# Kernel tuning notes

Hardware: AMD Instinct MI355X
Metric: run time of the kernel (lower is better)

Reference implementation:

```python
import jax, jax.numpy as jnp
import numpy as np

B, N, H, D, L = 4, 1024, 8, 256, 4
SVD, NSP = 16, 512
DK = D // H
EPS = 1e-6


def setup_inputs() -> dict:
    key = jax.random.key(0)
    ks = jax.random.split(key, 40)
    p = {}
    p["x"] = jax.random.normal(ks[0], (B, N, D), jnp.float32)
    p["in_degrees"] = jax.random.randint(ks[1], (N,), 0, N)
    p["out_degrees"] = jax.random.randint(ks[2], (N,), 0, N)
    p["spatial_pos"] = jax.random.randint(ks[3], (N, N), 0, NSP)
    p["svd_emb"] = jax.random.normal(ks[4], (N, 2 * SVD), jnp.float32)
    # embedding tables (padding_idx=0 -> zero row)
    p["in_deg_emb"] = (0.02 * jax.random.normal(ks[5], (N, D), jnp.float32)).at[0].set(0.0)
    p["out_deg_emb"] = (0.02 * jax.random.normal(ks[6], (N, D), jnp.float32)).at[0].set(0.0)
    p["spatial_emb"] = (0.02 * jax.random.normal(ks[7], (NSP, H), jnp.float32)).at[0].set(0.0)
    # SVD linear (stored [in, out]; y = x @ W + b)
    p["W_svd"] = 0.02 * jax.random.normal(ks[8], (2 * SVD, D), jnp.float32)
    p["b_svd"] = jnp.zeros((D,), jnp.float32)
    # per-layer stacked transformer params
    names = ["Wq", "Wk", "Wv", "Wa", "W1", "W2"]
    for i, nm in enumerate(names):
        p[nm] = 0.05 * jax.random.normal(ks[9 + i], (L, D, D), jnp.float32)
    for nm in ["bq", "bk", "bv", "ba", "b1", "b2", "ln1_b", "ln2_b"]:
        p[nm] = jnp.zeros((L, D), jnp.float32)
    p["ln1_g"] = jnp.ones((L, D), jnp.float32)
    p["ln2_g"] = jnp.ones((L, D), jnp.float32)
    return p


def _ln(x, g, b):
    mu = jnp.mean(x, axis=-1, keepdims=True)
    var = jnp.mean(jnp.square(x - mu), axis=-1, keepdims=True)
    return (x - mu) * jax.lax.rsqrt(var + EPS) * g + b


def _forward(x, svd_emb, W_svd, b_svd, in_deg_emb, out_deg_emb, spatial_emb,
             Wq, bq, Wk, bk, Wv, bv, Wa, ba, ln1_g, ln1_b,
             W1, b1, W2, b2, ln2_g, ln2_b,
             in_degrees, out_degrees, spatial_pos):
    # node-level: degree embeddings ([N,D] broadcasts over batch)
    x = x + in_deg_emb[in_degrees] + out_deg_emb[out_degrees]
    # node-level: SVD embedding (deterministic sign = +1 -> concat(u, -v))
    pos = jnp.concatenate([svd_emb[:, :SVD], -svd_emb[:, SVD:]], axis=-1)
    x = x + pos @ W_svd + b_svd
    # attention-level spatial bias: [N,N,H] -> [H,N,N], broadcast over batch
    attn_bias = jnp.transpose(spatial_emb[spatial_pos], (2, 0, 1))
    scale = 1.0 / jnp.sqrt(jnp.asarray(DK, x.dtype))

    def body(h, params):
        wq, bq_, wk, bk_, wv, bv_, wa, ba_, g1, b1_, w1, bb1, w2, bb2, g2, b2_ = params
        q = (h @ wq + bq_).reshape(B, N, H, DK)
        k = (h @ wk + bk_).reshape(B, N, H, DK)
        v = (h @ wv + bv_).reshape(B, N, H, DK)
        # scores [B,H,N,N] + spatial bias [H,N,N]
        scores = jnp.einsum('bqhd,bkhd->bhqk', q, k) * scale + attn_bias
        attn = jax.nn.softmax(scores, axis=-1)
        o = jnp.einsum('bhqk,bkhd->bqhd', attn, v).reshape(B, N, D)
        h = _ln(h + o @ wa + ba_, g1, b1_)
        f = jnp.maximum(h @ w1 + bb1, 0.0) @ w2 + bb2
        h = _ln(h + f, g2, b2_)
        return h, None

    x, _ = jax.lax.scan(body, x, (Wq, bq, Wk, bk, Wv, bv, Wa, ba, ln1_g, ln1_b,
                                  W1, b1, W2, b2, ln2_g, ln2_b))
    return x


def reference(x, svd_emb, W_svd, b_svd, in_deg_emb, out_deg_emb, spatial_emb,
              Wq, bq, Wk, bk, Wv, bv, Wa, ba, ln1_g, ln1_b,
              W1, b1, W2, b2, ln2_g, ln2_b,
              in_degrees, out_degrees, spatial_pos):
    return _forward(x, svd_emb, W_svd, b_svd, in_deg_emb, out_deg_emb, spatial_emb,
                    Wq, bq, Wk, bk, Wv, bv, Wa, ba, ln1_g, ln1_b,
                    W1, b1, W2, b2, ln2_g, ln2_b,
                    in_degrees, out_degrees, spatial_pos)
```

## Files before the change

### kernel.cpp

```cpp
#include <hip/hip_runtime.h>
#include <hip/hip_bf16.h>
#include <math.h>

#define NN 1024
#define BB 4
#define HH 8
#define DD 256
#define LL 4
#define DKK 32
#define MM 4096
#define EPSF 1e-6f

typedef __attribute__((ext_vector_type(8))) short short8;
typedef __attribute__((ext_vector_type(4))) float f32x4;

__device__ __forceinline__ unsigned short f2bf(float f) {
    __hip_bfloat16 h = __float2bfloat16(f);
    return *(unsigned short*)&h;
}
__device__ __forceinline__ float bf2f(unsigned short u) {
    unsigned v = ((unsigned)u) << 16;
    return __builtin_bit_cast(float, v);
}

__global__ __launch_bounds__(256) void init_kernel(
    const float* __restrict__ x, const int* __restrict__ deg_in,
    const int* __restrict__ deg_out, const float* __restrict__ svd,
    const float* __restrict__ in_emb, const float* __restrict__ out_emb,
    const float* __restrict__ Wsvd, const float* __restrict__ bsvd,
    const float* __restrict__ Wq, const float* __restrict__ Wk,
    const float* __restrict__ Wv, const float* __restrict__ Wa,
    const float* __restrict__ W1, const float* __restrict__ W2,
    const int* __restrict__ sp, const float* __restrict__ spemb,
    float* __restrict__ h, short* __restrict__ hb,
    short* __restrict__ Wt, short* __restrict__ bsw)
{
    int blk = blockIdx.x;
    int tid = threadIdx.x;
    {
        int n = blk & (NN - 1);
        int di = deg_in[n], dou = deg_out[n];
        float acc = x[(size_t)blk * DD + tid] + in_emb[(size_t)di * DD + tid]
                  + out_emb[(size_t)dou * DD + tid] + bsvd[tid];
        const float* sv = &svd[n * 32];
#pragma unroll
        for (int j = 0; j < 32; ++j) {
            float v = sv[j];
            v = (j < 16) ? v : -v;
            acc += v * Wsvd[j * DD + tid];
        }
        h[(size_t)blk * DD + tid] = acc;
        hb[(size_t)blk * DD + tid] = (short)f2bf(acc);
    }
    if (blk < 384) {
        __shared__ float t[64][65];
        int z = blk >> 4, tile = blk & 15;
        int name = z >> 2;
        const float* srcs[6] = {Wq, Wk, Wv, Wa, W1, W2};
        const float* W = srcs[name] + (size_t)(z & 3) * DD * DD;
        short* dst = Wt + (size_t)z * DD * DD;
        int r0 = (tile >> 2) * 64, c0 = (tile & 3) * 64;
#pragma unroll
        for (int i = 0; i < 16; ++i) {
            int idx = i * 256 + tid;
            int r = idx >> 6, cc = idx & 63;
            t[r][cc] = W[(size_t)(r0 + r) * DD + c0 + cc];
        }
        __syncthreads();
#pragma unroll
        for (int i = 0; i < 16; ++i) {
            int idx = i * 256 + tid;
            int n = idx >> 6, k = idx & 63;
            dst[(size_t)(c0 + n) * DD + r0 + k] = (short)f2bf(t[k][n]);
        }
    } else if (blk < 640) {
        int tt = (blk - 384) * 256 + tid;
        int ln = tt & 63, kt = (tt >> 6) & 15, q16 = tt >> 10;
        int qd = ln >> 4, cc = ln & 15;
        unsigned buf[8][8];
#pragma unroll
        for (int j = 0; j < 16; ++j) {
            int f = j >> 2, r = j & 3;
            int row = q16 * 16 + qd * 4 + r;
            int col = kt * 64 + f * 16 + cc;
            int pp = sp[row * NN + col];
#pragma unroll
            for (int hh = 0; hh < 8; ++hh) {
                unsigned short u = f2bf(spemb[pp * 8 + hh]);
                if (j & 1) buf[hh][j >> 1] |= ((unsigned)u) << 16;
                else       buf[hh][j >> 1] = u;
            }
        }
#pragma unroll
        for (int hh = 0; hh < 8; ++hh) {
            uint4* dst = (uint4*)&bsw[(((size_t)hh * 64 + q16) * 16 + kt) * 1024 + (size_t)ln * 16];
            dst[0] = make_uint4(buf[hh][0], buf[hh][1], buf[hh][2], buf[hh][3]);
            dst[1] = make_uint4(buf[hh][4], buf[hh][5], buf[hh][6], buf[hh][7]);
        }
    }
}

__global__ __launch_bounds__(256) void gemm_qkv_kernel(
    const short* __restrict__ A,
    const short* __restrict__ Wtq, const short* __restrict__ Wtk,
    const short* __restrict__ Wtv,
    const float* __restrict__ bq, const float* __restrict__ bk,
    const float* __restrict__ bv,
    short* __restrict__ qo, short* __restrict__ ko, short* __restrict__ vo)
{
    int z = blockIdx.z;
    const short* Wt = (z == 0) ? Wtq : (z == 1) ? Wtk : Wtv;
    const float* bs = (z == 0) ? bq : (z == 1) ? bk : bv;
    int tid = threadIdx.x, wave = tid >> 6, lane = tid & 63;
    int quad = lane >> 4, c = lane & 15;
    int m0 = blockIdx.x * 16;
    int n0 = blockIdx.y * 64 + wave * 16;
    f32x4 acc = {0.f, 0.f, 0.f, 0.f};
    const short* Ap = &A[(size_t)(m0 + c) * DD];
#pragma unroll
    for (int ks = 0; ks < 8; ++ks) {
        short8 af = *(const short8*)&Ap[ks * 32 + quad * 8];
        short8 bf = *(const short8*)&Wt[(size_t)(n0 + c) * DD + ks * 32 + quad * 8];
        acc = __builtin_amdgcn_mfma_f32_16x16x32_bf16(af, bf, acc, 0, 0, 0);
    }
    int b = m0 >> 10;
    int tok0 = (m0 & (NN - 1)) + quad * 4;
    int col = n0 + c;
    int head = col >> 5, dk = col & 31;
    int bh = b * 8 + head;
    float bv2 = bs[col];
    const float scale = 0.17677669529663687f;
    if (z == 2) {
        ushort4 pk;
        pk.x = f2bf(acc[0] + bv2); pk.y = f2bf(acc[1] + bv2);
        pk.z = f2bf(acc[2] + bv2); pk.w = f2bf(acc[3] + bv2);
        *(ushort4*)&vo[((size_t)bh * DKK + dk) * NN + tok0] = pk;
    } else {
        short* out = (z == 0) ? qo : ko;
        float sc = (z == 0) ? scale : 1.0f;
#pragma unroll
        for (int r = 0; r < 4; ++r)
            out[((size_t)bh * NN + tok0 + r) * DKK + dk] =
                (short)f2bf((acc[r] + bv2) * sc);
    }
}

template <int QKV>
__global__ __launch_bounds__(512) void layer_kernel(
    const short* __restrict__ q, const short* __restrict__ k,
    const short* __restrict__ vt, const short* __restrict__ bsw,
    const short* __restrict__ Wta, const short* __restrict__ Wt1,
    const short* __restrict__ Wt2,
    const float* __restrict__ ba, const float* __restrict__ b1,
    const float* __restrict__ b2,
    const float* __restrict__ g1, const float* __restrict__ lb1,
    const float* __restrict__ g2, const float* __restrict__ lb2,
    float* __restrict__ h,
    const short* __restrict__ Wtqn, const short* __restrict__ Wtkn,
    const short* __restrict__ Wtvn,
    const float* __restrict__ bqn, const float* __restrict__ bkn,
    const float* __restrict__ bvn,
    short* __restrict__ qo, short* __restrict__ ko, short* __restrict__ vo)
{
    int tid = threadIdx.x, wave = tid >> 6, lane = tid & 63;
    int quad = lane >> 4, c = lane & 15;
    int m0 = blockIdx.x * 16;
    int b = m0 >> 10;
    int q0 = m0 & (NN - 1);
    int qt_idx = q0 >> 4;
    int head = wave;
    int bh = b * 8 + head;
    int nb = wave * 32;

    __shared__ short Pl[8][16][72];
    __shared__ short t_in[16][264];
    __shared__ short t1s[16][264];
    __shared__ float shs[8][16][2];
    const f32x4 zero = {0.f, 0.f, 0.f, 0.f};

    {
        short (*P)[72] = Pl[wave];
        short8 qf = *(const short8*)&q[((size_t)bh * NN + q0 + c) * DKK + quad * 8];
        f32x4 Oa0 = zero, Oa1 = zero;
        float lsum[4] = {0.f, 0.f, 0.f, 0.f};

        short8 kf[4];
#pragma unroll
        for (int f = 0; f < 4; ++f)
            kf[f] = *(const short8*)&k[((size_t)bh * NN + f * 16 + c) * DKK + quad * 8];

        for (int kti = 0; kti < 16; ++kti) {
            int kt = kti * 64;
            f32x4 s[4];
#pragma unroll
            for (int f = 0; f < 4; ++f)
                s[f] = __builtin_amdgcn_mfma_f32_16x16x32_bf16(qf, kf[f], zero, 0, 0, 0);
            if (kti < 15) {
#pragma unroll
                for (int f = 0; f < 4; ++f)
                    kf[f] = *(const short8*)&k[((size_t)bh * NN + kt + 64 + f * 16 + c) * DKK + quad * 8];
            }
            short8 vf0[2], vf1[2];
#pragma unroll
            for (int kc = 0; kc < 2; ++kc) {
                vf0[kc] = *(const short8*)&vt[((size_t)bh * DKK + 0  + c) * NN + kt + kc * 32 + quad * 8];
                vf1[kc] = *(const short8*)&vt[((size_t)bh * DKK + 16 + c) * NN + kt + kc * 32 + quad * 8];
            }
            const short* bp = &bsw[(((size_t)head * 64 + qt_idx) * 16 + kti) * 1024 + (size_t)lane * 16];
            short8 b0 = *(const short8*)bp;
            short8 b1v = *(const short8*)(bp + 8);
#pragma unroll
            for (int f = 0; f < 4; ++f)
#pragma unroll
                for (int r = 0; r < 4; ++r) {
                    int jj = f * 4 + r;
                    unsigned short uu = (unsigned short)((jj < 8) ? b0[jj] : b1v[jj - 8]);
                    float p = __expf(s[f][r] + bf2f(uu));
                    s[f][r] = p;
                    lsum[r] += p;
                }
#pragma unroll
            for (int f = 0; f < 4; ++f)
#pragma unroll
                for (int r = 0; r < 4; ++r)
                    P[quad * 4 + r][f * 16 + c] = (short)f2bf(s[f][r]);
#pragma unroll
            for (int kc = 0; kc < 2; ++kc) {
                short8 pf = *(const short8*)&P[c][kc * 32 + quad * 8];
                Oa0 = __builtin_amdgcn_mfma_f32_16x16x32_bf16(pf, vf0[kc], Oa0, 0, 0, 0);
                Oa1 = __builtin_amdgcn_mfma_f32_16x16x32_bf16(pf, vf1[kc], Oa1, 0, 0, 0);
            }
        }
#pragma unroll
        for (int r = 0; r < 4; ++r)
#pragma unroll
            for (int off = 1; off < 16; off <<= 1)
                lsum[r] += __shfl_xor(lsum[r], off);
#pragma unroll
        for (int r = 0; r < 4; ++r) {
            float invl = 1.0f / lsum[r];
            int rr = quad * 4 + r;
            t_in[rr][head * 32 + c]      = (short)f2bf(Oa0[r] * invl);
            t_in[rr][head * 32 + 16 + c] = (short)f2bf(Oa1[r] * invl);
        }
    }
    __syncthreads();

    f32x4 acc[2] = {zero, zero};
#pragma unroll
    for (int ks = 0; ks < 8; ++ks) {
        short8 af = *(const short8*)&t_in[c][ks * 32 + quad * 8];
#pragma unroll
        for (int f = 0; f < 2; ++f) {
            short8 bf = *(const short8*)&Wta[(size_t)(nb + f * 16 + c) * DD + ks * 32 + quad * 8];
            acc[f] = __builtin_amdgcn_mfma_f32_16x16x32_bf16(af, bf, acc[f], 0, 0, 0);
        }
    }
    float val[2][4];
    float ps[4] = {0.f,0.f,0.f,0.f}, ps2[4] = {0.f,0.f,0.f,0.f};
#pragma unroll
    for (int f = 0; f < 2; ++f) {
        int col = nb + f * 16 + c;
        float bv = ba[col];
#pragma unroll
        for (int r = 0; r < 4; ++r) {
            float v = h[(size_t)(m0 + quad * 4 + r) * DD + col] + acc[f][r] + bv;
            val[f][r] = v;
            ps[r] += v;
            ps2[r] += v * v;
        }
    }
#pragma unroll
    for (int r = 0; r < 4; ++r)
#pragma unroll
        for (int off = 1; off < 16; off <<= 1) {
            ps[r]  += __shfl_xor(ps[r], off);
            ps2[r] += __shfl_xor(ps2[r], off);
        }
    if (c == 0)
#pragma unroll
        for (int r = 0; r < 4; ++r) {
            shs[wave][quad * 4 + r][0] = ps[r];
            shs[wave][quad * 4 + r][1] = ps2[r];
        }
    __syncthreads();
    float res[2][4];
#pragma unroll
    for (int r = 0; r < 4; ++r) {
        int rr = quad * 4 + r;
        float ts = 0.f, t2 = 0.f;
#pragma unroll
        for (int w = 0; w < 8; ++w) { ts += shs[w][rr][0]; t2 += shs[w][rr][1]; }
        float mu = ts * (1.0f / DD);
        float rv = rsqrtf(t2 * (1.0f / DD) - mu * mu + EPSF);
#pragma unroll
        for (int f = 0; f < 2; ++f) {
            int col = nb + f * 16 + c;
            float nv = (val[f][r] - mu) * rv * g1[col] + lb1[col];
            res[f][r] = nv;
            t_in[rr][col] = (short)f2bf(nv);
        }
    }
    __syncthreads();
#pragma unroll
    for (int f = 0; f < 2; ++f) {
        int n0 = nb + f * 16;
        f32x4 a1 = zero;
#pragma unroll
        for (int ks = 0; ks < 8; ++ks) {
            short8 af = *(const short8*)&t_in[c][ks * 32 + quad * 8];
            short8 bf = *(const short8*)&Wt1[(size_t)(n0 + c) * DD + ks * 32 + quad * 8];
            a1 = __builtin_amdgcn_mfma_f32_16x16x32_bf16(af, bf, a1, 0, 0, 0);
        }
        float bv = b1[n0 + c];
#pragma unroll
        for (int r = 0; r < 4; ++r)
            t1s[quad * 4 + r][n0 + c] = (short)f2bf(fmaxf(a1[r] + bv, 0.f));
    }
    __syncthreads();
    f32x4 acc2[2] = {zero, zero};
#pragma unroll
    for (int ks = 0; ks < 8; ++ks) {
        short8 af = *(const short8*)&t1s[c][ks * 32 + quad * 8];
#pragma unroll
        for (int f = 0; f < 2; ++f) {
            short8 bf = *(const short8*)&Wt2[(size_t)(nb + f * 16 + c) * DD + ks * 32 + quad * 8];
            acc2[f] = __builtin_amdgcn_mfma_f32_16x16x32_bf16(af, bf, acc2[f], 0, 0, 0);
        }
    }
    float ps_2[4] = {0.f,0.f,0.f,0.f}, ps2_2[4] = {0.f,0.f,0.f,0.f};
#pragma unroll
    for (int f = 0; f < 2; ++f) {
        int col = nb + f * 16 + c;
        float bv = b2[col];
#pragma unroll
        for (int r = 0; r < 4; ++r) {
            float v = res[f][r] + acc2[f][r] + bv;
            val[f][r] = v;
            ps_2[r] += v;
            ps2_2[r] += v * v;
        }
    }
#pragma unroll
    for (int r = 0; r < 4; ++r)
#pragma unroll
        for (int off = 1; off < 16; off <<= 1) {
            ps_2[r]  += __shfl_xor(ps_2[r], off);
            ps2_2[r] += __shfl_xor(ps2_2[r], off);
        }
    __syncthreads();
    if (c == 0)
#pragma unroll
        for (int r = 0; r < 4; ++r) {
            shs[wave][quad * 4 + r][0] = ps_2[r];
            shs[wave][quad * 4 + r][1] = ps2_2[r];
        }
    __syncthreads();
#pragma unroll
    for (int r = 0; r < 4; ++r) {
        int rr = quad * 4 + r;
        float ts = 0.f, t2 = 0.f;
#pragma unroll
        for (int w = 0; w < 8; ++w) { ts += shs[w][rr][0]; t2 += shs[w][rr][1]; }
        float mu = ts * (1.0f / DD);
        float rv = rsqrtf(t2 * (1.0f / DD) - mu * mu + EPSF);
#pragma unroll
        for (int f = 0; f < 2; ++f) {
            int col = nb + f * 16 + c;
            float nv = (val[f][r] - mu) * rv * g2[col] + lb2[col];
            h[(size_t)(m0 + rr) * DD + col] = nv;
            t_in[rr][col] = (short)f2bf(nv);
        }
    }
    if (QKV == 0) return;
    __syncthreads();
    {
        int tok0 = q0 + quad * 4;
        const short* Wz[3]  = {Wtqn, Wtkn, Wtvn};
        const float* bz[3]  = {bqn, bkn, bvn};
        const float scale = 0.17677669529663687f;
#pragma unroll
        for (int z = 0; z < 3; ++z) {
#pragma unroll
            for (int f = 0; f < 2; ++f) {
                int n0 = nb + f * 16;
                f32x4 aq = zero;
#pragma unroll
                for (int ks = 0; ks < 8; ++ks) {
                    short8 af = *(const short8*)&t_in[c][ks * 32 + quad * 8];
                    short8 bf = *(const short8*)&Wz[z][(size_t)(n0 + c) * DD + ks * 32 + quad * 8];
                    aq = __builtin_amdgcn_mfma_f32_16x16x32_bf16(af, bf, aq, 0, 0, 0);
                }
                int col = n0 + c;
                int hd = col >> 5, dk = col & 31;
                int bh2 = b * 8 + hd;
                float bv2 = bz[z][col];
                if (z == 2) {
                    ushort4 pk;
                    pk.x = f2bf(aq[0] + bv2); pk.y = f2bf(aq[1] + bv2);
                    pk.z = f2bf(aq[2] + bv2); pk.w = f2bf(aq[3] + bv2);
                    *(ushort4*)&vo[((size_t)bh2 * DKK + dk) * NN + tok0] = pk;
                } else {
                    short* out = (z == 0) ? qo : ko;
                    float sc = (z == 0) ? scale : 1.0f;
#pragma unroll
                    for (int r = 0; r < 4; ++r)
                        out[((size_t)bh2 * NN + tok0 + r) * DKK + dk] =
                            (short)f2bf((aq[r] + bv2) * sc);
                }
            }
        }
    }
}

extern "C" void kernel_launch(void* const* d_in, const int* in_sizes, int n_in,
                              void* d_out, int out_size, void* d_ws, size_t ws_size,
                              hipStream_t stream)
{
    const float* x       = (const float*)d_in[0];
    const int*   deg_in  = (const int*)d_in[1];
    const int*   deg_out = (const int*)d_in[2];
    const int*   sp      = (const int*)d_in[3];
    const float* svd     = (const float*)d_in[4];
    const float* in_emb  = (const float*)d_in[5];
    const float* out_emb = (const float*)d_in[6];
    const float* spemb   = (const float*)d_in[7];
    const float* Wsvd    = (const float*)d_in[8];
    const float* bsvd    = (const float*)d_in[9];
    const float* Wq = (const float*)d_in[10];
    const float* Wk = (const float*)d_in[11];
    const float* Wv = (const float*)d_in[12];
    const float* Wa = (const float*)d_in[13];
    const float* W1 = (const float*)d_in[14];
    const float* W2 = (const float*)d_in[15];
    const float* bq = (const float*)d_in[16];
    const float* bk = (const float*)d_in[17];
    const float* bv = (const float*)d_in[18];
    const float* ba = (const float*)d_in[19];
    const float* b1 = (const float*)d_in[20];
    const float* b2 = (const float*)d_in[21];
    const float* ln1b = (const float*)d_in[22];
    const float* ln2b = (const float*)d_in[23];
    const float* ln1g = (const float*)d_in[24];
    const float* ln2g = (const float*)d_in[25];

    float* h = (float*)d_out;
    char*  ws = (char*)d_ws;
    short* bias = (short*)ws;
    short* qb   = (short*)(ws + ((size_t)16 << 20));
    short* kb   = (short*)(ws + ((size_t)18 << 20));
    short* vtb  = (short*)(ws + ((size_t)20 << 20));
    short* hb   = (short*)(ws + ((size_t)26 << 20));
    short* Wt   = (short*)(ws + ((size_t)28 << 20));

    init_kernel<<<MM, 256, 0, stream>>>(x, deg_in, deg_out, svd, in_emb,
        out_emb, Wsvd, bsvd, Wq, Wk, Wv, Wa, W1, W2, sp, spemb, h, hb, Wt, bias);

    const size_t WSZ = (size_t)DD * DD;
    gemm_qkv_kernel<<<dim3(MM / 16, 4, 3), 256, 0, stream>>>(
        hb, Wt + 0 * WSZ, Wt + 4 * WSZ, Wt + 8 * WSZ, bq, bk, bv, qb, kb, vtb);

    for (int l = 0; l < LL; ++l) {
        const size_t bo = (size_t)l * DD;
        const short* Wta = Wt + (3 * 4 + l) * WSZ;
        const short* Wt1 = Wt + (4 * 4 + l) * WSZ;
        const short* Wt2 = Wt + (5 * 4 + l) * WSZ;

        if (l < LL - 1) {
            const size_t bo_n = (size_t)(l + 1) * DD;
            layer_kernel<1><<<MM / 16, 512, 0, stream>>>(
                qb, kb, vtb, bias, Wta, Wt1, Wt2,
                ba + bo, b1 + bo, b2 + bo,
                ln1g + bo, ln1b + bo, ln2g + bo, ln2b + bo, h,
                Wt + (0 * 4 + l + 1) * WSZ, Wt + (1 * 4 + l + 1) * WSZ,
                Wt + (2 * 4 + l + 1) * WSZ,
                bq + bo_n, bk + bo_n, bv + bo_n, qb, kb, vtb);
        } else {
            layer_kernel<0><<<MM / 16, 512, 0, stream>>>(
                qb, kb, vtb, bias, Wta, Wt1, Wt2,
                ba + bo, b1 + bo, b2 + bo,
                ln1g + bo, ln1b + bo, ln2g + bo, ln2b + bo, h,
                nullptr, nullptr, nullptr, nullptr, nullptr, nullptr,
                nullptr, nullptr, nullptr);
        }
    }
}
```

Measured before the change: 345.8 us.

## Split attention key range across two waves per head and use exp2

Doubles the layer kernel block to 1024 threads so each head's key range is split between two waves, whose partial outputs and row sums are combined through shared memory. The downstream GEMMs now give each wave a single 16-column tile. Scores are pre-scaled by log2(e) in the q projection and bias table so exp2 can replace expf, and the bias loads are double-buffered. This adds more parallelism per 16-row tile at the cost of an extra shared-memory reduction and barrier, and possible register-pressure limits at 1024 threads.

Measured after the change: 356.9 us. +3.2%, slower.

```diff
diff --git a/kernel.cpp b/kernel.cpp
--- a/kernel.cpp
+++ b/kernel.cpp
@@ -10,6 +10,8 @@
 #define DKK 32
 #define MM 4096
 #define EPSF 1e-6f
+#define LOG2EF 1.4426950408889634f
+#define SCLOG2E 0.2550348625f
 
 typedef __attribute__((ext_vector_type(8))) short short8;
 typedef __attribute__((ext_vector_type(4))) float f32x4;
@@ -70,8 +72,8 @@
 #pragma unroll
         for (int i = 0; i < 16; ++i) {
             int idx = i * 256 + tid;
-            int n = idx >> 6, k = idx & 63;
-            dst[(size_t)(c0 + n) * DD + r0 + k] = (short)f2bf(t[k][n]);
+            int n = idx >> 6, kk = idx & 63;
+            dst[(size_t)(c0 + n) * DD + r0 + kk] = (short)f2bf(t[kk][n]);
         }
     } else if (blk < 640) {
         int tt = (blk - 384) * 256 + tid;
@@ -82,11 +84,14 @@
         for (int j = 0; j < 16; ++j) {
             int f = j >> 2, r = j & 3;
             int row = q16 * 16 + qd * 4 + r;
-            int col = kt * 64 + f * 16 + cc;
-            int pp = sp[row * NN + col];
+            int colj = kt * 64 + f * 16 + cc;
+            int pp = sp[row * NN + colj];
+            float4 e0 = *(const float4*)&spemb[pp * 8];
+            float4 e1 = *(const float4*)&spemb[pp * 8 + 4];
+            float ev[8] = {e0.x, e0.y, e0.z, e0.w, e1.x, e1.y, e1.z, e1.w};
 #pragma unroll
             for (int hh = 0; hh < 8; ++hh) {
-                unsigned short u = f2bf(spemb[pp * 8 + hh]);
+                unsigned short u = f2bf(ev[hh] * LOG2EF);
                 if (j & 1) buf[hh][j >> 1] |= ((unsigned)u) << 16;
                 else       buf[hh][j >> 1] = u;
             }
@@ -129,7 +134,6 @@
     int head = col >> 5, dk = col & 31;
     int bh = b * 8 + head;
     float bv2 = bs[col];
-    const float scale = 0.17677669529663687f;
     if (z == 2) {
         ushort4 pk;
         pk.x = f2bf(acc[0] + bv2); pk.y = f2bf(acc[1] + bv2);
@@ -137,7 +141,7 @@
         *(ushort4*)&vo[((size_t)bh * DKK + dk) * NN + tok0] = pk;
     } else {
         short* out = (z == 0) ? qo : ko;
-        float sc = (z == 0) ? scale : 1.0f;
+        float sc = (z == 0) ? SCLOG2E : 1.0f;
 #pragma unroll
         for (int r = 0; r < 4; ++r)
             out[((size_t)bh * NN + tok0 + r) * DKK + dk] =
@@ -146,7 +150,7 @@
 }
 
 template <int QKV>
-__global__ __launch_bounds__(512) void layer_kernel(
+__global__ __launch_bounds__(1024) void layer_kernel(
     const short* __restrict__ q, const short* __restrict__ k,
     const short* __restrict__ vt, const short* __restrict__ bsw,
     const short* __restrict__ Wta, const short* __restrict__ Wt1,
@@ -168,34 +172,40 @@
     int b = m0 >> 10;
     int q0 = m0 & (NN - 1);
     int qt_idx = q0 >> 4;
-    int head = wave;
+    int head = wave >> 1;
+    int khalf = wave & 1;
     int bh = b * 8 + head;
-    int nb = wave * 32;
-
-    __shared__ short Pl[8][16][72];
+    int nb = wave * 16;
+
+    __shared__ short Pl[16][16][72];
     __shared__ short t_in[16][264];
     __shared__ short t1s[16][264];
-    __shared__ float shs[8][16][2];
+    __shared__ float shs[16][16][2];
     const f32x4 zero = {0.f, 0.f, 0.f, 0.f};
+
+    f32x4 Oa0 = zero, Oa1 = zero;
+    float lsum[4] = {0.f, 0.f, 0.f, 0.f};
 
     {
         short (*P)[72] = Pl[wave];
         short8 qf = *(const short8*)&q[((size_t)bh * NN + q0 + c) * DKK + quad * 8];
-        f32x4 Oa0 = zero, Oa1 = zero;
-        float lsum[4] = {0.f, 0.f, 0.f, 0.f};
+        const int kt0 = khalf * 8;
 
         short8 kf[4];
 #pragma unroll
         for (int f = 0; f < 4; ++f)
-            kf[f] = *(const short8*)&k[((size_t)bh * NN + f * 16 + c) * DKK + quad * 8];
-
-        for (int kti = 0; kti < 16; ++kti) {
+            kf[f] = *(const short8*)&k[((size_t)bh * NN + kt0 * 64 + f * 16 + c) * DKK + quad * 8];
+        const short* bpc = &bsw[(((size_t)head * 64 + qt_idx) * 16 + kt0) * 1024 + (size_t)lane * 16];
+        short8 bc0 = *(const short8*)bpc;
+        short8 bc1 = *(const short8*)(bpc + 8);
+
+        for (int kti = kt0; kti < kt0 + 8; ++kti) {
             int kt = kti * 64;
             f32x4 s[4];
 #pragma unroll
             for (int f = 0; f < 4; ++f)
                 s[f] = __builtin_amdgcn_mfma_f32_16x16x32_bf16(qf, kf[f], zero, 0, 0, 0);
-            if (kti < 15) {
+            if (kti < kt0 + 7) {
 #pragma unroll
                 for (int f = 0; f < 4; ++f)
                     kf[f] = *(const short8*)&k[((size_t)bh * NN + kt + 64 + f * 16 + c) * DKK + quad * 8];
@@ -206,19 +216,23 @@
                 vf0[kc] = *(const short8*)&vt[((size_t)bh * DKK + 0  + c) * NN + kt + kc * 32 + quad * 8];
                 vf1[kc] = *(const short8*)&vt[((size_t)bh * DKK + 16 + c) * NN + kt + kc * 32 + quad * 8];
             }
-            const short* bp = &bsw[(((size_t)head * 64 + qt_idx) * 16 + kti) * 1024 + (size_t)lane * 16];
-            short8 b0 = *(const short8*)bp;
-            short8 b1v = *(const short8*)(bp + 8);
+            short8 bn0 = bc0, bn1 = bc1;
+            if (kti < kt0 + 7) {
+                const short* bp = &bsw[(((size_t)head * 64 + qt_idx) * 16 + kti + 1) * 1024 + (size_t)lane * 16];
+                bn0 = *(const short8*)bp;
+                bn1 = *(const short8*)(bp + 8);
+            }
 #pragma unroll
             for (int f = 0; f < 4; ++f)
 #pragma unroll
                 for (int r = 0; r < 4; ++r) {
                     int jj = f * 4 + r;
-                    unsigned short uu = (unsigned short)((jj < 8) ? b0[jj] : b1v[jj - 8]);
-                    float p = __expf(s[f][r] + bf2f(uu));
+                    unsigned short uu = (unsigned short)((jj < 8) ? bc0[jj] : bc1[jj - 8]);
+                    float p = __builtin_amdgcn_exp2f(s[f][r] + bf2f(uu));
                     s[f][r] = p;
                     lsum[r] += p;
                 }
+            bc0 = bn0; bc1 = bn1;
 #pragma unroll
             for (int f = 0; f < 4; ++f)
 #pragma unroll
@@ -236,38 +250,50 @@
 #pragma unroll
             for (int off = 1; off < 16; off <<= 1)
                 lsum[r] += __shfl_xor(lsum[r], off);
+        if (khalf) {
+            float* Ob = (float*)Pl[wave];
+#pragma unroll
+            for (int r = 0; r < 4; ++r) {
+                int rr = quad * 4 + r;
+                Ob[rr * 32 + c]      = Oa0[r];
+                Ob[rr * 32 + 16 + c] = Oa1[r];
+            }
+            if (c == 0)
+#pragma unroll
+                for (int r = 0; r < 4; ++r)
+                    shs[wave][quad * 4 + r][0] = lsum[r];
+        }
+    }
+    __syncthreads();
+    if (!khalf) {
+        const float* Ob = (const float*)Pl[wave + 1];
 #pragma unroll
         for (int r = 0; r < 4; ++r) {
-            float invl = 1.0f / lsum[r];
             int rr = quad * 4 + r;
-            t_in[rr][head * 32 + c]      = (short)f2bf(Oa0[r] * invl);
-            t_in[rr][head * 32 + 16 + c] = (short)f2bf(Oa1[r] * invl);
-        }
-    }
-    __syncthreads();
-
-    f32x4 acc[2] = {zero, zero};
+            float invl = 1.0f / (lsum[r] + shs[wave + 1][rr][0]);
+            t_in[rr][head * 32 + c]      = (short)f2bf((Oa0[r] + Ob[rr * 32 + c]) * invl);
+            t_in[rr][head * 32 + 16 + c] = (short)f2bf((Oa1[r] + Ob[rr * 32 + 16 + c]) * invl);
+        }
+    }
+    __syncthreads();
+
+    int col = nb + c;
+    f32x4 acc = zero;
 #pragma unroll
     for (int ks = 0; ks < 8; ++ks) {
         short8 af = *(const short8*)&t_in[c][ks * 32 + quad * 8];
-#pragma unroll
-        for (int f = 0; f < 2; ++f) {
-            short8 bf = *(const short8*)&Wta[(size_t)(nb + f * 16 + c) * DD + ks * 32 + quad * 8];
-            acc[f] = __builtin_amdgcn_mfma_f32_16x16x32_bf16(af, bf, acc[f], 0, 0, 0);
-        }
-    }
-    float val[2][4];
-    float ps[4] = {0.f,0.f,0.f,0.f}, ps2[4] = {0.f,0.f,0.f,0.f};
-#pragma unroll
-    for (int f = 0; f < 2; ++f) {
-        int col = nb + f * 16 + c;
-        float bv = ba[col];
+        short8 bf = *(const short8*)&Wta[(size_t)col * DD + ks * 32 + quad * 8];
+        acc = __builtin_amdgcn_mfma_f32_16x16x32_bf16(af, bf, acc, 0, 0, 0);
+    }
+    float val[4], ps[4], ps2[4];
+    {
+        float bvv = ba[col];
 #pragma unroll
         for (int r = 0; r < 4; ++r) {
-            float v = h[(size_t)(m0 + quad * 4 + r) * DD + col] + acc[f][r] + bv;
-            val[f][r] = v;
-            ps[r] += v;
-            ps2[r] += v * v;
+            float v = h[(size_t)(m0 + quad * 4 + r) * DD + col] + acc[r] + bvv;
+            val[r] = v;
+            ps[r] = v;
+            ps2[r] = v * v;
         }
     }
 #pragma unroll
@@ -284,76 +310,63 @@
             shs[wave][quad * 4 + r][1] = ps2[r];
         }
     __syncthreads();
-    float res[2][4];
+    float res[4];
 #pragma unroll
     for (int r = 0; r < 4; ++r) {
         int rr = quad * 4 + r;
         float ts = 0.f, t2 = 0.f;
 #pragma unroll
-        for (int w = 0; w < 8; ++w) { ts += shs[w][rr][0]; t2 += shs[w][rr][1]; }
+        for (int w = 0; w < 16; ++w) { ts += shs[w][rr][0]; t2 += shs[w][rr][1]; }
         float mu = ts * (1.0f / DD);
         float rv = rsqrtf(t2 * (1.0f / DD) - mu * mu + EPSF);
-#pragma unroll
-        for (int f = 0; f < 2; ++f) {
-            int col = nb + f * 16 + c;
-            float nv = (val[f][r] - mu) * rv * g1[col] + lb1[col];
-            res[f][r] = nv;
-            t_in[rr][col] = (short)f2bf(nv);
-        }
-    }
-    __syncthreads();
-#pragma unroll
-    for (int f = 0; f < 2; ++f) {
-        int n0 = nb + f * 16;
-        f32x4 a1 = zero;
-#pragma unroll
-        for (int ks = 0; ks < 8; ++ks) {
-            short8 af = *(const short8*)&t_in[c][ks * 32 + quad * 8];
-            short8 bf = *(const short8*)&Wt1[(size_t)(n0 + c) * DD + ks * 32 + quad * 8];
-            a1 = __builtin_amdgcn_mfma_f32_16x16x32_bf16(af, bf, a1, 0, 0, 0);
-        }
-        float bv = b1[n0 + c];
+        float nv = (val[r] - mu) * rv * g1[col] + lb1[col];
+        res[r] = nv;
+        t_in[rr][col] = (short)f2bf(nv);
+    }
+    __syncthreads();
+    f32x4 a1 = zero;
+#pragma unroll
+    for (int ks = 0; ks < 8; ++ks) {
+        short8 af = *(const short8*)&t_in[c][ks * 32 + quad * 8];
+        short8 bf = *(const short8*)&Wt1[(size_t)col * DD + ks * 32 + quad * 8];
+        a1 = __builtin_amdgcn_mfma_f32_16x16x32_bf16(af, bf, a1, 0, 0, 0);
+    }
+    {
+        float bvv = b1[col];
 #pragma unroll
         for (int r = 0; r < 4; ++r)
-            t1s[quad * 4 + r][n0 + c] = (short)f2bf(fmaxf(a1[r] + bv, 0.f));
-    }
-    __syncthreads();
-    f32x4 acc2[2] = {zero, zero};
+            t1s[quad * 4 + r][col] = (short)f2bf(fmaxf(a1[r] + bvv, 0.f));
+    }
+    __syncthreads();
+    f32x4 a2 = zero;
 #pragma unroll
     for (int ks = 0; ks < 8; ++ks) {
         short8 af = *(const short8*)&t1s[c][ks * 32 + quad * 8];
-#pragma unroll
-        for (int f = 0; f < 2; ++f) {
-            short8 bf = *(const short8*)&Wt2[(size_t)(nb + f * 16 + c) * DD + ks * 32 + quad * 8];
-            acc2[f] = __builtin_amdgcn_mfma_f32_16x16x32_bf16(af, bf, acc2[f], 0, 0, 0);
-        }
-    }
-    float ps_2[4] = {0.f,0.f,0.f,0.f}, ps2_2[4] = {0.f,0.f,0.f,0.f};
-#pragma unroll
-    for (int f = 0; f < 2; ++f) {
-        int col = nb + f * 16 + c;
-        float bv = b2[col];
+        short8 bf = *(const short8*)&Wt2[(size_t)col * DD + ks * 32 + quad * 8];
+        a2 = __builtin_amdgcn_mfma_f32_16x16x32_bf16(af, bf, a2, 0, 0, 0);
+    }
+    {
+        float bvv = b2[col];
 #pragma unroll
         for (int r = 0; r < 4; ++r) {
-            float v = res[f][r] + acc2[f][r] + bv;
-            val[f][r] = v;
-            ps_2[r] += v;
-            ps2_2[r] += v * v;
+            float v = res[r] + a2[r] + bvv;
+            val[r] = v;
+            ps[r] = v;
+            ps2[r] = v * v;
         }
     }
 #pragma unroll
     for (int r = 0; r < 4; ++r)
 #pragma unroll
         for (int off = 1; off < 16; off <<= 1) {
-            ps_2[r]  += __shfl_xor(ps_2[r], off);
-            ps2_2[r] += __shfl_xor(ps2_2[r], off);
-        }
-    __syncthreads();
+            ps[r]  += __shfl_xor(ps[r], off);
+            ps2[r] += __shfl_xor(ps2[r], off);
+        }
     if (c == 0)
 #pragma unroll
         for (int r = 0; r < 4; ++r) {
-            shs[wave][quad * 4 + r][0] = ps_2[r];
-            shs[wave][quad * 4 + r][1] = ps2_2[r];
+            shs[wave][quad * 4 + r][0] = ps[r];
+            shs[wave][quad * 4 + r][1] = ps2[r];
         }
     __syncthreads();
 #pragma unroll
@@ -361,53 +374,43 @@
         int rr = quad * 4 + r;
         float ts = 0.f, t2 = 0.f;
 #pragma unroll
-        for (int w = 0; w < 8; ++w) { ts += shs[w][rr][0]; t2 += shs[w][rr][1]; }
+        for (int w = 0; w < 16; ++w) { ts += shs[w][rr][0]; t2 += shs[w][rr][1]; }
         float mu = ts * (1.0f / DD);
         float rv = rsqrtf(t2 * (1.0f / DD) - mu * mu + EPSF);
-#pragma unroll
-        for (int f = 0; f < 2; ++f) {
-            int col = nb + f * 16 + c;
-            float nv = (val[f][r] - mu) * rv * g2[col] + lb2[col];
-            h[(size_t)(m0 + rr) * DD + col] = nv;
-            t_in[rr][col] = (short)f2bf(nv);
-        }
+        float nv = (val[r] - mu) * rv * g2[col] + lb2[col];
+        h[(size_t)(m0 + rr) * DD + col] = nv;
+        t_in[rr][col] = (short)f2bf(nv);
     }
     if (QKV == 0) return;
     __syncthreads();
     {
         int tok0 = q0 + quad * 4;
-        const short* Wz[3]  = {Wtqn, Wtkn, Wtvn};
-        const float* bz[3]  = {bqn, bkn, bvn};
-        const float scale = 0.17677669529663687f;
+        const short* Wz[3] = {Wtqn, Wtkn, Wtvn};
+        const float* bz[3] = {bqn, bkn, bvn};
 #pragma unroll
         for (int z = 0; z < 3; ++z) {
-#pragma unroll
-            for (int f = 0; f < 2; ++f) {
-                int n0 = nb + f * 16;
-                f32x4 aq = zero;
-#pragma unroll
-                for (int ks = 0; ks < 8; ++ks) {
-                    short8 af = *(const short8*)&t_in[c][ks * 32 + quad * 8];
-                    short8 bf = *(const short8*)&Wz[z][(size_t)(n0 + c) * DD + ks * 32 + quad * 8];
-                    aq = __builtin_amdgcn_mfma_f32_16x16x32_bf16(af, bf, aq, 0, 0, 0);
-                }
-                int col = n0 + c;
-                int hd = col >> 5, dk = col & 31;
-                int bh2 = b * 8 + hd;
-                float bv2 = bz[z][col];
-                if (z == 2) {
-                    ushort4 pk;
-                    pk.x = f2bf(aq[0] + bv2); pk.y = f2bf(aq[1] + bv2);
-                    pk.z = f2bf(aq[2] + bv2); pk.w = f2bf(aq[3] + bv2);
-                    *(ushort4*)&vo[((size_t)bh2 * DKK + dk) * NN + tok0] = pk;
-                } else {
-                    short* out = (z == 0) ? qo : ko;
-                    float sc = (z == 0) ? scale : 1.0f;
-#pragma unroll
-                    for (int r = 0; r < 4; ++r)
-                        out[((size_t)bh2 * NN + tok0 + r) * DKK + dk] =
-                            (short)f2bf((aq[r] + bv2) * sc);
-                }
+            f32x4 aq = zero;
+#pragma unroll
+            for (int ks = 0; ks < 8; ++ks) {
+                short8 af = *(const short8*)&t_in[c][ks * 32 + quad * 8];
+                short8 bf = *(const short8*)&Wz[z][(size_t)col * DD + ks * 32 + quad * 8];
+                aq = __builtin_amdgcn_mfma_f32_16x16x32_bf16(af, bf, aq, 0, 0, 0);
+            }
+            int hd = col >> 5, dk = col & 31;
+            int bh2 = b * 8 + hd;
+            float bvv = bz[z][col];
+            if (z == 2) {
+                ushort4 pk;
+                pk.x = f2bf(aq[0] + bvv); pk.y = f2bf(aq[1] + bvv);
+                pk.z = f2bf(aq[2] + bvv); pk.w = f2bf(aq[3] + bvv);
+                *(ushort4*)&vo[((size_t)bh2 * DKK + dk) * NN + tok0] = pk;
+            } else {
+                short* out = (z == 0) ? qo : ko;
+                float sc = (z == 0) ? SCLOG2E : 1.0f;
+#pragma unroll
+                for (int r = 0; r < 4; ++r)
+                    out[((size_t)bh2 * NN + tok0 + r) * DKK + dk] =
+                        (short)f2bf((aq[r] + bvv) * sc);
             }
         }
     }
@@ -468,7 +471,7 @@
 
         if (l < LL - 1) {
             const size_t bo_n = (size_t)(l + 1) * DD;
-            layer_kernel<1><<<MM / 16, 512, 0, stream>>>(
+            layer_kernel<1><<<MM / 16, 1024, 0, stream>>>(
                 qb, kb, vtb, bias, Wta, Wt1, Wt2,
                 ba + bo, b1 + bo, b2 + bo,
                 ln1g + bo, ln1b + bo, ln2g + bo, ln2b + bo, h,
@@ -476,7 +479,7 @@
                 Wt + (2 * 4 + l + 1) * WSZ,
                 bq + bo_n, bk + bo_n, bv + bo_n, qb, kb, vtb);
         } else {
-            layer_kernel<0><<<MM / 16, 512, 0, stream>>>(
+            layer_kernel<0><<<MM / 16, 1024, 0, stream>>>(
                 qb, kb, vtb, bias, Wta, Wt1, Wt2,
                 ba + bo, b1 + bo, b2 + bo,
                 ln1g + bo, ln1b + bo, ln2g + bo, ln2b + bo, h,
```

## Split layer kernel into half-tile blocks, use exp2 softmax, prefetch bias

Applied to the files above, without the earlier changes.

The fused layer kernel now launches twice as many blocks. Each block owns 8 query rows, duplicated into the 16-row MFMA tile, and only half the lanes write results. This is meant to put more waves on each CU and hide memory latency better, at the cost of redundant MFMA work and repeated weight loads. Separately, log2(e) is folded into the Q scale and into the spatial bias table so the softmax can use the hardware exp2 instead of __expf. The next key tile's bias fragment is also prefetched one iteration ahead.

Result: slower. 504.9 us (+46.0%).

```diff
diff --git a/kernel.cpp b/kernel.cpp
--- a/kernel.cpp
+++ b/kernel.cpp
@@ -10,6 +10,8 @@
 #define DKK 32
 #define MM 4096
 #define EPSF 1e-6f
+#define LOG2EF 1.4426950408889634f
+#define SCLOG2E 0.2550348625f
 
 typedef __attribute__((ext_vector_type(8))) short short8;
 typedef __attribute__((ext_vector_type(4))) float f32x4;
@@ -70,8 +72,8 @@
 #pragma unroll
         for (int i = 0; i < 16; ++i) {
             int idx = i * 256 + tid;
-            int n = idx >> 6, k = idx & 63;
-            dst[(size_t)(c0 + n) * DD + r0 + k] = (short)f2bf(t[k][n]);
+            int n = idx >> 6, kk = idx & 63;
+            dst[(size_t)(c0 + n) * DD + r0 + kk] = (short)f2bf(t[kk][n]);
         }
     } else if (blk < 640) {
         int tt = (blk - 384) * 256 + tid;
@@ -82,11 +84,14 @@
         for (int j = 0; j < 16; ++j) {
             int f = j >> 2, r = j & 3;
             int row = q16 * 16 + qd * 4 + r;
-            int col = kt * 64 + f * 16 + cc;
-            int pp = sp[row * NN + col];
+            int colj = kt * 64 + f * 16 + cc;
+            int pp = sp[row * NN + colj];
+            float4 e0 = *(const float4*)&spemb[pp * 8];
+            float4 e1 = *(const float4*)&spemb[pp * 8 + 4];
+            float ev[8] = {e0.x, e0.y, e0.z, e0.w, e1.x, e1.y, e1.z, e1.w};
 #pragma unroll
             for (int hh = 0; hh < 8; ++hh) {
-                unsigned short u = f2bf(spemb[pp * 8 + hh]);
+                unsigned short u = f2bf(ev[hh] * LOG2EF);
                 if (j & 1) buf[hh][j >> 1] |= ((unsigned)u) << 16;
                 else       buf[hh][j >> 1] = u;
             }
@@ -129,7 +134,6 @@
     int head = col >> 5, dk = col & 31;
     int bh = b * 8 + head;
     float bv2 = bs[col];
-    const float scale = 0.17677669529663687f;
     if (z == 2) {
         ushort4 pk;
         pk.x = f2bf(acc[0] + bv2); pk.y = f2bf(acc[1] + bv2);
@@ -137,7 +141,7 @@
         *(ushort4*)&vo[((size_t)bh * DKK + dk) * NN + tok0] = pk;
     } else {
         short* out = (z == 0) ? qo : ko;
-        float sc = (z == 0) ? scale : 1.0f;
+        float sc = (z == 0) ? SCLOG2E : 1.0f;
 #pragma unroll
         for (int r = 0; r < 4; ++r)
             out[((size_t)bh * NN + tok0 + r) * DKK + dk] =
@@ -164,9 +168,14 @@
 {
     int tid = threadIdx.x, wave = tid >> 6, lane = tid & 63;
     int quad = lane >> 4, c = lane & 15;
-    int m0 = blockIdx.x * 16;
+    int bx = blockIdx.x;
+    int qt = bx & 255;
+    int half = bx >> 8;
+    int m0 = qt * 16;
+    int m0h = m0 + half * 8;
     int b = m0 >> 10;
     int q0 = m0 & (NN - 1);
+    int q0h = q0 + half * 8;
     int qt_idx = q0 >> 4;
     int head = wave;
     int bh = b * 8 + head;
@@ -178,9 +187,11 @@
     __shared__ float shs[8][16][2];
     const f32x4 zero = {0.f, 0.f, 0.f, 0.f};
 
+    int bl = (half * 2 + (quad & 1)) * 16 + c;
+
     {
         short (*P)[72] = Pl[wave];
-        short8 qf = *(const short8*)&q[((size_t)bh * NN + q0 + c) * DKK + quad * 8];
+        short8 qf = *(const short8*)&q[((size_t)bh * NN + q0h + (c & 7)) * DKK + quad * 8];
         f32x4 Oa0 = zero, Oa1 = zero;
         float lsum[4] = {0.f, 0.f, 0.f, 0.f};
 
@@ -188,6 +199,9 @@
 #pragma unroll
         for (int f = 0; f < 4; ++f)
             kf[f] = *(const short8*)&k[((size_t)bh * NN + f * 16 + c) * DKK + quad * 8];
+        const short* bbase = &bsw[(((size_t)head * 64 + qt_idx) * 16) * 1024 + (size_t)bl * 16];
+        short8 bc0 = *(const short8*)bbase;
+        short8 bc1 = *(const short8*)(bbase + 8);
 
         for (int kti = 0; kti < 16; ++kti) {
             int kt = kti * 64;
@@ -206,19 +220,23 @@
                 vf0[kc] = *(const short8*)&vt[((size_t)bh * DKK + 0  + c) * NN + kt + kc * 32 + quad * 8];
                 vf1[kc] = *(const short8*)&vt[((size_t)bh * DKK + 16 + c) * NN + kt + kc * 32 + quad * 8];
             }
-            const short* bp = &bsw[(((size_t)head * 64 + qt_idx) * 16 + kti) * 1024 + (size_t)lane * 16];
-            short8 b0 = *(const short8*)bp;
-            short8 b1v = *(const short8*)(bp + 8);
+            short8 bn0 = bc0, bn1 = bc1;
+            if (kti < 15) {
+                const short* bp = bbase + (size_t)(kti + 1) * 1024;
+                bn0 = *(const short8*)bp;
+                bn1 = *(const short8*)(bp + 8);
+            }
 #pragma unroll
             for (int f = 0; f < 4; ++f)
 #pragma unroll
                 for (int r = 0; r < 4; ++r) {
                     int jj = f * 4 + r;
-                    unsigned short uu = (unsigned short)((jj < 8) ? b0[jj] : b1v[jj - 8]);
-                    float p = __expf(s[f][r] + bf2f(uu));
+                    unsigned short uu = (unsigned short)((jj < 8) ? bc0[jj] : bc1[jj - 8]);
+                    float p = __builtin_amdgcn_exp2f(s[f][r] + bf2f(uu));
                     s[f][r] = p;
                     lsum[r] += p;
                 }
+            bc0 = bn0; bc1 = bn1;
 #pragma unroll
             for (int f = 0; f < 4; ++f)
 #pragma unroll
@@ -264,7 +282,7 @@
         float bv = ba[col];
 #pragma unroll
         for (int r = 0; r < 4; ++r) {
-            float v = h[(size_t)(m0 + quad * 4 + r) * DD + col] + acc[f][r] + bv;
+            float v = h[(size_t)(m0h + ((quad * 4 + r) & 7)) * DD + col] + acc[f][r] + bv;
             val[f][r] = v;
             ps[r] += v;
             ps2[r] += v * v;
@@ -368,17 +386,17 @@
         for (int f = 0; f < 2; ++f) {
             int col = nb + f * 16 + c;
             float nv = (val[f][r] - mu) * rv * g2[col] + lb2[col];
-            h[(size_t)(m0 + rr) * DD + col] = nv;
+            if (quad < 2)
+                h[(size_t)(m0h + rr) * DD + col] = nv;
             t_in[rr][col] = (short)f2bf(nv);
         }
     }
     if (QKV == 0) return;
     __syncthreads();
     {
-        int tok0 = q0 + quad * 4;
-        const short* Wz[3]  = {Wtqn, Wtkn, Wtvn};
-        const float* bz[3]  = {bqn, bkn, bvn};
-        const float scale = 0.17677669529663687f;
+        int tok0 = q0h + quad * 4;
+        const short* Wz[3] = {Wtqn, Wtkn, Wtvn};
+        const float* bz[3] = {bqn, bkn, bvn};
 #pragma unroll
         for (int z = 0; z < 3; ++z) {
 #pragma unroll
@@ -391,22 +409,24 @@
                     short8 bf = *(const short8*)&Wz[z][(size_t)(n0 + c) * DD + ks * 32 + quad * 8];
                     aq = __builtin_amdgcn_mfma_f32_16x16x32_bf16(af, bf, aq, 0, 0, 0);
                 }
-                int col = n0 + c;
-                int hd = col >> 5, dk = col & 31;
-                int bh2 = b * 8 + hd;
-                float bv2 = bz[z][col];
-                if (z == 2) {
-                    ushort4 pk;
-                    pk.x = f2bf(aq[0] + bv2); pk.y = f2bf(aq[1] + bv2);
-                    pk.z = f2bf(aq[2] + bv2); pk.w = f2bf(aq[3] + bv2);
-                    *(ushort4*)&vo[((size_t)bh2 * DKK + dk) * NN + tok0] = pk;
-                } else {
-                    short* out = (z == 0) ? qo : ko;
-                    float sc = (z == 0) ? scale : 1.0f;
-#pragma unroll
-                    for (int r = 0; r < 4; ++r)
-                        out[((size_t)bh2 * NN + tok0 + r) * DKK + dk] =
-                            (short)f2bf((aq[r] + bv2) * sc);
+                if (quad < 2) {
+                    int col = n0 + c;
+                    int hd = col >> 5, dk = col & 31;
+                    int bh2 = b * 8 + hd;
+                    float bv2 = bz[z][col];
+                    if (z == 2) {
+                        ushort4 pk;
+                        pk.x = f2bf(aq[0] + bv2); pk.y = f2bf(aq[1] + bv2);
+                        pk.z = f2bf(aq[2] + bv2); pk.w = f2bf(aq[3] + bv2);
+                        *(ushort4*)&vo[((size_t)bh2 * DKK + dk) * NN + tok0] = pk;
+                    } else {
+                        short* out = (z == 0) ? qo : ko;
+                        float sc = (z == 0) ? SCLOG2E : 1.0f;
+#pragma unroll
+                        for (int r = 0; r < 4; ++r)
+                            out[((size_t)bh2 * NN + tok0 + r) * DKK + dk] =
+                                (short)f2bf((aq[r] + bv2) * sc);
+                    }
                 }
             }
         }
@@ -468,7 +488,7 @@
 
         if (l < LL - 1) {
             const size_t bo_n = (size_t)(l + 1) * DD;
-            layer_kernel<1><<<MM / 16, 512, 0, stream>>>(
+            layer_kernel<1><<<2 * (MM / 16), 512, 0, stream>>>(
                 qb, kb, vtb, bias, Wta, Wt1, Wt2,
                 ba + bo, b1 + bo, b2 + bo,
                 ln1g + bo, ln1b + bo, ln2g + bo, ln2b + bo, h,
@@ -476,7 +496,7 @@
                 Wt + (2 * 4 + l + 1) * WSZ,
                 bq + bo_n, bk + bo_n, bv + bo_n, qb, kb, vtb);
         } else {
-            layer_kernel<0><<<MM / 16, 512, 0, stream>>>(
+            layer_kernel<0><<<2 * (MM / 16), 512, 0, stream>>>(
                 qb, kb, vtb, bias, Wta, Wt1, Wt2,
                 ba + bo, b1 + bo, b2 + bo,
                 ln1g + bo, ln1b + bo, ln2g + bo, ln2b + bo, h,
```
